# Optimization experiments

Hardware: AMD Instinct MI355X
Metric: run time of the kernel (lower is better)

## Reference

```python
import jax, jax.numpy as jnp
import numpy as np
import math

D_MODEL = 1024
N_HEADS = 16
SPARSITY = 0.3


def setup_inputs() -> dict:
    key = jax.random.key(0)
    ks = jax.random.split(key, 12)
    B, S, D = 4, 2048, D_MODEL
    Dh = D // 2
    sc = 0.02
    inp = {
        "x": jax.random.normal(ks[0], (B, S, D), dtype=jnp.float32),
        "wq": jax.random.normal(ks[1], (D, D), dtype=jnp.float32) * sc,
        "bq": jnp.zeros((D,), jnp.float32),
        "wk": jax.random.normal(ks[2], (D, D), dtype=jnp.float32) * sc,
        "bk": jnp.zeros((D,), jnp.float32),
        "wv": jax.random.normal(ks[3], (D, D), dtype=jnp.float32) * sc,
        "bv": jnp.zeros((D,), jnp.float32),
        "wo": jax.random.normal(ks[4], (D, D), dtype=jnp.float32) * sc,
        "bo": jnp.zeros((D,), jnp.float32),
        "wi1": jax.random.normal(ks[5], (Dh, D), dtype=jnp.float32) * sc,
        "bi1": jnp.zeros((Dh,), jnp.float32),
        "wi2": jax.random.normal(ks[6], (1, Dh), dtype=jnp.float32) * sc,
        "bi2": jnp.zeros((1,), jnp.float32),
    }
    return inp


def reference(x, wq, bq, wk, bk, wv, bv, wo, bo, wi1, bi1, wi2, bi2):
    B, S, D = x.shape
    H = N_HEADS
    hd = D // H
    k = max(1, int(S * SPARSITY))

    # projections (torch Linear: x @ W^T + b)
    Q = (x @ wq.T + bq).reshape(B, S, H, hd).transpose(0, 2, 1, 3)  # [B,H,S,hd]
    K = (x @ wk.T + bk).reshape(B, S, H, hd).transpose(0, 2, 1, 3)
    V = (x @ wv.T + bv).reshape(B, S, H, hd).transpose(0, 2, 1, 3)

    # learned indexer -> per-position importance [B,S]
    h = jnp.maximum(x @ wi1.T + bi1, 0.0)
    importance = (h @ wi2.T + bi2)[..., 0]

    _, top_idx = jax.lax.top_k(importance, k)  # [B,k]
    sparse_mask = jnp.zeros((B, S), dtype=x.dtype).at[
        jnp.arange(B)[:, None], top_idx
    ].set(1.0)

    scores = jnp.einsum("bhqd,bhkd->bhqk", Q, K) / math.sqrt(hd)
    scores = jnp.where(sparse_mask[:, None, None, :] == 0, -jnp.inf, scores)
    attn = jax.nn.softmax(scores, axis=-1)

    out = jnp.einsum("bhqk,bhkd->bhqd", attn, V)
    out = out.transpose(0, 2, 1, 3).reshape(B, S, D)
    return out @ wo.T + bo
```

## Files before the change

kernel.cpp:

```cpp
#include <hip/hip_runtime.h>
#include <math.h>

#define BB 4
#define SS 2048
#define DD 1024
#define HHD 16
#define HD 64
#define DH 512
#define KSEL 614
#define KPAD 640
#define MTOT (BB*SS)
#define QKVS 3072
#define NCH (KPAD/64)

typedef __attribute__((ext_vector_type(8))) short bf16x8;
typedef __attribute__((ext_vector_type(4))) float f32x4;

#define LDS_CAST(p) ((__attribute__((address_space(3))) void*)(p))
#define GLB_CAST(p) ((const __attribute__((address_space(1))) void*)(p))

__device__ inline short bf16rne(float v)
{
    unsigned u = __builtin_bit_cast(unsigned, v);
    return (short)((u + 0x7FFFu + ((u >> 16) & 1u)) >> 16);
}

__device__ inline void split1(float v, short& h, short& l)
{
    unsigned u = __builtin_bit_cast(unsigned, v);
    unsigned hr = (u + 0x7FFFu + ((u >> 16) & 1u)) >> 16;
    h = (short)hr;
    float hf = __builtin_bit_cast(float, hr << 16);
    float res = v - hf;
    unsigned u2 = __builtin_bit_cast(unsigned, res);
    unsigned lr = (u2 + 0x7FFFu + ((u2 >> 16) & 1u)) >> 16;
    l = (short)lr;
}

__global__ __launch_bounds__(256)
void split_convert(const float* __restrict__ in, short* __restrict__ hi,
                   short* __restrict__ lo, int n4)
{
    const int i = blockIdx.x * 256 + threadIdx.x;
    if (i >= n4) return;
    float4 v = reinterpret_cast<const float4*>(in)[i];
    short4 h, l;
    split1(v.x, h.x, l.x);
    split1(v.y, h.y, l.y);
    split1(v.z, h.z, l.z);
    split1(v.w, h.w, l.w);
    reinterpret_cast<short4*>(hi)[i] = h;
    reinterpret_cast<short4*>(lo)[i] = l;
}

__global__ __launch_bounds__(256)
void split_weights(const float* __restrict__ wq, const float* __restrict__ wk,
                   const float* __restrict__ wv, const float* __restrict__ wo,
                   const float* __restrict__ wi1,
                   short* __restrict__ Bqkv_hi, short* __restrict__ wo_hi,
                   short* __restrict__ Wi_hi, short* __restrict__ Wi_lo)
{
    const int i = blockIdx.x * 256 + threadIdx.x;
    const int which = blockIdx.y;
    if (which < 4) {
        const float* src = (which == 0) ? wq : (which == 1) ? wk : (which == 2) ? wv : wo;
        short* dst = (which == 3) ? wo_hi : (Bqkv_hi + (size_t)which * DD * DD);
        float4 v = reinterpret_cast<const float4*>(src)[i];
        short4 hh;
        hh.x = bf16rne(v.x); hh.y = bf16rne(v.y); hh.z = bf16rne(v.z); hh.w = bf16rne(v.w);
        reinterpret_cast<short4*>(dst)[i] = hh;
    } else {
        if (i >= DH*DD/4) return;
        float4 v = reinterpret_cast<const float4*>(wi1)[i];
        short4 h, l;
        split1(v.x, h.x, l.x); split1(v.y, h.y, l.y);
        split1(v.z, h.z, l.z); split1(v.w, h.w, l.w);
        reinterpret_cast<short4*>(Wi_hi)[i] = h;
        reinterpret_cast<short4*>(Wi_lo)[i] = l;
    }
}

__global__ __launch_bounds__(256)
void concat_bias3(const float* __restrict__ a, const float* __restrict__ b,
                  const float* __restrict__ c, float* __restrict__ o)
{
    const int i = blockIdx.x * 256 + threadIdx.x;
    o[i] = (i < 1024) ? a[i] : ((i < 2048) ? b[i - 1024] : c[i - 2048]);
}

template<bool BF16_OUT, bool QSCALE>
__global__ __launch_bounds__(256)
void gemm_bf16(const short* __restrict__ Ahi, const short* __restrict__ Bhi,
               const float* __restrict__ bias, void* __restrict__ Cv,
               int M, int N, int K, int ldc)
{
    __shared__ short sAh[128*64];
    __shared__ short sBh[128*64];

    const int t = threadIdx.x;
    const int lane = t & 63, wid = t >> 6;
    const int wm = wid >> 1, wn = wid & 1;
    const int row0 = blockIdx.y * 128, col0 = blockIdx.x * 128;
    const int g = lane >> 4, r = lane & 15;
    const int lrow = lane >> 3;
    const int lslot = lane & 7;

    f32x4 acc[4][4];
    #pragma unroll
    for (int mt = 0; mt < 4; ++mt)
        #pragma unroll
        for (int nt = 0; nt < 4; ++nt) acc[mt][nt] = (f32x4){0.f, 0.f, 0.f, 0.f};

    for (int k0 = 0; k0 < K; k0 += 64) {
        #pragma unroll
        for (int e = 0; e < 4; ++e) {
            const int rl = wid * 32 + e * 8 + lrow;
            const int scol = k0 + ((lslot ^ (rl & 7)) << 3);
            const size_t ga = (size_t)(row0 + rl) * K + scol;
            const size_t gb = (size_t)(col0 + rl) * K + scol;
            const int ldso = (wid * 32 + e * 8) * 64;
            __builtin_amdgcn_global_load_lds(GLB_CAST(Ahi + ga), LDS_CAST(sAh + ldso), 16, 0, 0);
            __builtin_amdgcn_global_load_lds(GLB_CAST(Bhi + gb), LDS_CAST(sBh + ldso), 16, 0, 0);
        }
        __syncthreads();

        #pragma unroll
        for (int kk = 0; kk < 2; ++kk) {
            bf16x8 ah[4], bh[4];
            #pragma unroll
            for (int mt = 0; mt < 4; ++mt) {
                const int rw = wm * 64 + mt * 16 + r;
                ah[mt] = *reinterpret_cast<const bf16x8*>(sAh + rw * 64 + (((kk*4 + g) ^ (rw & 7)) << 3));
            }
            #pragma unroll
            for (int nt = 0; nt < 4; ++nt) {
                const int rw = wn * 64 + nt * 16 + r;
                bh[nt] = *reinterpret_cast<const bf16x8*>(sBh + rw * 64 + (((kk*4 + g) ^ (rw & 7)) << 3));
            }
            #pragma unroll
            for (int mt = 0; mt < 4; ++mt)
                #pragma unroll
                for (int nt = 0; nt < 4; ++nt)
                    acc[mt][nt] = __builtin_amdgcn_mfma_f32_16x16x32_bf16(ah[mt], bh[nt], acc[mt][nt], 0, 0, 0);
        }
        __syncthreads();
    }

    #pragma unroll
    for (int nt = 0; nt < 4; ++nt) {
        const int col = wn * 64 + nt * 16 + r;
        const float bv = bias[col0 + col];
        const bool qs = QSCALE && (col0 + col) < 1024;
        #pragma unroll
        for (int mt = 0; mt < 4; ++mt) {
            #pragma unroll
            for (int e = 0; e < 4; ++e) {
                const int row = row0 + wm * 64 + mt * 16 + 4 * g + e;
                float v = acc[mt][nt][e] + bv;
                if (qs) v *= 0.125f;
                if (BF16_OUT)
                    ((short*)Cv)[(size_t)row * ldc + col0 + col] = bf16rne(v);
                else
                    ((float*)Cv)[(size_t)row * ldc + col0 + col] = v;
            }
        }
    }
}

template<bool RELU>
__global__ __launch_bounds__(256)
void gemm_split(const short* __restrict__ Ahi, const short* __restrict__ Alo,
                const short* __restrict__ Bhi, const short* __restrict__ Blo,
                const float* __restrict__ bias, float* __restrict__ C,
                int M, int N, int K, int ldc)
{
    __shared__ short sAh[128*32];
    __shared__ short sAl[128*32];
    __shared__ short sBh[128*32];
    __shared__ short sBl[128*32];

    const int t = threadIdx.x;
    const int lane = t & 63, wid = t >> 6;
    const int wm = wid >> 1, wn = wid & 1;
    const int row0 = blockIdx.y * 128, col0 = blockIdx.x * 128;
    const int g = lane >> 4, r = lane & 15;
    const int sw = g ^ ((lane >> 2) & 3);
    const int srow = lane >> 2;
    const int sslot = lane & 3;

    f32x4 acc[4][4];
    #pragma unroll
    for (int mt = 0; mt < 4; ++mt)
        #pragma unroll
        for (int nt = 0; nt < 4; ++nt) acc[mt][nt] = (f32x4){0.f, 0.f, 0.f, 0.f};

    for (int k0 = 0; k0 < K; k0 += 32) {
        #pragma unroll
        for (int i = 0; i < 2; ++i) {
            const int rl = wid * 32 + i * 16 + srow;
            const int scol = k0 + ((sslot ^ ((rl >> 2) & 3)) << 3);
            const size_t ga = (size_t)(row0 + rl) * K + scol;
            const size_t gb = (size_t)(col0 + rl) * K + scol;
            const int ldso = (wid * 32 + i * 16) * 32;
            __builtin_amdgcn_global_load_lds(GLB_CAST(Ahi + ga), LDS_CAST(sAh + ldso), 16, 0, 0);
            __builtin_amdgcn_global_load_lds(GLB_CAST(Alo + ga), LDS_CAST(sAl + ldso), 16, 0, 0);
            __builtin_amdgcn_global_load_lds(GLB_CAST(Bhi + gb), LDS_CAST(sBh + ldso), 16, 0, 0);
            __builtin_amdgcn_global_load_lds(GLB_CAST(Blo + gb), LDS_CAST(sBl + ldso), 16, 0, 0);
        }
        __syncthreads();

        bf16x8 ah[4], al[4], bh[4], bl[4];
        #pragma unroll
        for (int mt = 0; mt < 4; ++mt) {
            const int row = wm * 64 + mt * 16 + r;
            ah[mt] = *reinterpret_cast<const bf16x8*>(sAh + row * 32 + sw * 8);
            al[mt] = *reinterpret_cast<const bf16x8*>(sAl + row * 32 + sw * 8);
        }
        #pragma unroll
        for (int nt = 0; nt < 4; ++nt) {
            const int row = wn * 64 + nt * 16 + r;
            bh[nt] = *reinterpret_cast<const bf16x8*>(sBh + row * 32 + sw * 8);
            bl[nt] = *reinterpret_cast<const bf16x8*>(sBl + row * 32 + sw * 8);
        }
        #pragma unroll
        for (int mt = 0; mt < 4; ++mt)
            #pragma unroll
            for (int nt = 0; nt < 4; ++nt) {
                acc[mt][nt] = __builtin_amdgcn_mfma_f32_16x16x32_bf16(ah[mt], bh[nt], acc[mt][nt], 0, 0, 0);
                acc[mt][nt] = __builtin_amdgcn_mfma_f32_16x16x32_bf16(ah[mt], bl[nt], acc[mt][nt], 0, 0, 0);
                acc[mt][nt] = __builtin_amdgcn_mfma_f32_16x16x32_bf16(al[mt], bh[nt], acc[mt][nt], 0, 0, 0);
            }
        __syncthreads();
    }

    #pragma unroll
    for (int nt = 0; nt < 4; ++nt) {
        const int col = wn * 64 + nt * 16 + r;
        const float bv = bias[col0 + col];
        #pragma unroll
        for (int mt = 0; mt < 4; ++mt) {
            #pragma unroll
            for (int e = 0; e < 4; ++e) {
                const int row = row0 + wm * 64 + mt * 16 + 4 * g + e;
                float v = acc[mt][nt][e] + bv;
                if (RELU) v = fmaxf(v, 0.f);
                C[(size_t)row * ldc + col0 + col] = v;
            }
        }
    }
}

__global__ __launch_bounds__(256)
void importance_kernel(const float* __restrict__ h, const float* __restrict__ wi2,
                       const float* __restrict__ bi2, float* __restrict__ imp)
{
    const int wid = threadIdx.x >> 6, lane = threadIdx.x & 63;
    const int row = blockIdx.x * 4 + wid;
    const float* hr = h + (size_t)row * DH;
    float s = 0.f;
    #pragma unroll
    for (int i = 0; i < DH/64; ++i)
        s = fmaf(hr[lane + i*64], wi2[lane + i*64], s);
    #pragma unroll
    for (int off = 32; off; off >>= 1) s += __shfl_down(s, off);
    if (lane == 0) imp[row] = s + bi2[0];
}

__global__ __launch_bounds__(256)
void rank_kernel(const float* __restrict__ imp, int* __restrict__ flags)
{
    __shared__ float simp[SS];
    const int b = blockIdx.y;
    const int t = threadIdx.x;
    const float* bimp = imp + b * SS;
    for (int i = t; i < SS/4; i += 256)
        reinterpret_cast<float4*>(simp)[i] = reinterpret_cast<const float4*>(bimp)[i];
    __syncthreads();

    const int i = blockIdx.x * 32 + (t >> 3);
    const int part = t & 7;
    const float v = simp[i];
    const float4* slice = reinterpret_cast<const float4*>(simp + part * (SS/8));
    const int jb = part * (SS/8);
    int rank = 0;
    #pragma unroll 8
    for (int jj = 0; jj < SS/32; ++jj) {
        const float4 u4 = slice[jj];
        const int j = jb + jj * 4;
        rank += (u4.x > v) || ((u4.x == v) && (j + 0 < i));
        rank += (u4.y > v) || ((u4.y == v) && (j + 1 < i));
        rank += (u4.z > v) || ((u4.z == v) && (j + 2 < i));
        rank += (u4.w > v) || ((u4.w == v) && (j + 3 < i));
    }
    rank += __shfl_xor(rank, 1);
    rank += __shfl_xor(rank, 2);
    rank += __shfl_xor(rank, 4);
    if (part == 0) flags[b * SS + i] = (rank < KSEL) ? 1 : 0;
}

__global__ __launch_bounds__(256)
void compact_kernel(const int* __restrict__ flags, int* __restrict__ idxg)
{
    __shared__ int sscan[SS];
    __shared__ int sidx[KSEL];
    const int b = blockIdx.x, t = threadIdx.x;
    for (int i = t; i < SS; i += 256) sscan[i] = flags[b * SS + i];
    __syncthreads();
    for (int off = 1; off < SS; off <<= 1) {
        int vals[SS/256];
        #pragma unroll
        for (int c = 0; c < SS/256; ++c) {
            const int i = t + c * 256;
            int v = sscan[i];
            if (i >= off) v += sscan[i - off];
            vals[c] = v;
        }
        __syncthreads();
        #pragma unroll
        for (int c = 0; c < SS/256; ++c) sscan[t + c * 256] = vals[c];
        __syncthreads();
    }
    for (int i = t; i < SS; i += 256) {
        const int f = flags[b * SS + i];
        if (f) sidx[sscan[i] - 1] = i;
    }
    __syncthreads();
    for (int p = t; p < KPAD; p += 256)
        idxg[b * KPAD + p] = sidx[min(p, KSEL - 1)];
}

__global__ __launch_bounds__(256)
void gather_kv(const short* __restrict__ QKVb, const int* __restrict__ idxg,
               short* __restrict__ Kg, short* __restrict__ Vg)
{
    __shared__ short Vs[64*72];
    const int t = threadIdx.x;
    const int c = blockIdx.x, h = blockIdx.y, b = blockIdx.z;
    const int srow = t >> 2;
    const int sq4  = t & 3;

    const size_t cbase = ((size_t)(b * HHD + h) * NCH + c) * 4096;

    const int krow = idxg[b * KPAD + c * 64 + srow];
    const short* kb = QKVb + (size_t)(b * SS + krow) * QKVS + 1024 + h * HD + sq4 * 16;
    bf16x8 k0 = *reinterpret_cast<const bf16x8*>(kb);
    bf16x8 k1 = *reinterpret_cast<const bf16x8*>(kb + 8);
    short* kout = Kg + cbase + srow * HD + sq4 * 16;
    *reinterpret_cast<bf16x8*>(kout)     = k0;
    *reinterpret_cast<bf16x8*>(kout + 8) = k1;

    const short* vbp = kb + 1024;
    bf16x8 v0 = *reinterpret_cast<const bf16x8*>(vbp);
    bf16x8 v1 = *reinterpret_cast<const bf16x8*>(vbp + 8);
    #pragma unroll
    for (int j = 0; j < 8; ++j) {
        Vs[(sq4 * 16 + j) * 72 + srow]     = v0[j];
        Vs[(sq4 * 16 + 8 + j) * 72 + srow] = v1[j];
    }
    __syncthreads();

    const int x = 8 * (srow >> 4);
    short* vout = Vg + cbase + srow * 64;
    *reinterpret_cast<bf16x8*>(vout + ((sq4 * 16)     ^ x)) = *reinterpret_cast<const bf16x8*>(&Vs[srow * 72 + sq4 * 16]);
    *reinterpret_cast<bf16x8*>(vout + ((sq4 * 16 + 8) ^ x)) = *reinterpret_cast<const bf16x8*>(&Vs[srow * 72 + sq4 * 16 + 8]);
}

__global__ __launch_bounds__(256)
void attn_mfma(const short* __restrict__ QKVb, const short* __restrict__ Kg,
               const short* __restrict__ Vg, short* __restrict__ AOhi)
{
    __shared__ short Ks[2][64*72];
    __shared__ short Vs[2][64*72];
    __shared__ short Ps[4][16*72];

    const int t = threadIdx.x;
    const int lane = t & 63, w = t >> 6;
    const int g = lane >> 4, r = lane & 15;
    const int qt = blockIdx.x, h = blockIdx.y, b = blockIdx.z;
    const int q0 = qt * 64;
    short* Psw = &Ps[w][0];

    const int srow = t >> 2;
    const int scol = (t & 3) * 16;
    const short* kcbase = Kg + ((size_t)(b * HHD + h) * NCH) * 4096 + srow * 64 + scol;
    const short* vcbase = Vg + ((size_t)(b * HHD + h) * NCH) * 4096 + srow * 64 + scol;

    bf16x8 qh[2];
    {
        const short* qrow = QKVb + (size_t)(b * SS + q0 + w * 16 + r) * QKVS + h * HD;
        qh[0] = *reinterpret_cast<const bf16x8*>(qrow + 8 * g);
        qh[1] = *reinterpret_cast<const bf16x8*>(qrow + 32 + 8 * g);
    }

    bf16x8 ones;
    #pragma unroll
    for (int j = 0; j < 8; ++j) ones[j] = (short)0x3F80;

    f32x4 oacc[4];
    #pragma unroll
    for (int dt = 0; dt < 4; ++dt) oacc[dt] = (f32x4){0.f, 0.f, 0.f, 0.f};
    f32x4 dacc = (f32x4){0.f, 0.f, 0.f, 0.f};

    bf16x8 kreg0 = *reinterpret_cast<const bf16x8*>(kcbase);
    bf16x8 kreg1 = *reinterpret_cast<const bf16x8*>(kcbase + 8);
    bf16x8 vreg0 = *reinterpret_cast<const bf16x8*>(vcbase);
    bf16x8 vreg1 = *reinterpret_cast<const bf16x8*>(vcbase + 8);

    for (int c = 0; c < NCH; ++c) {
        const int cur = c & 1;
        *reinterpret_cast<bf16x8*>(&Ks[cur][srow*72 + scol])     = kreg0;
        *reinterpret_cast<bf16x8*>(&Ks[cur][srow*72 + scol + 8]) = kreg1;
        *reinterpret_cast<bf16x8*>(&Vs[cur][srow*72 + scol])     = vreg0;
        *reinterpret_cast<bf16x8*>(&Vs[cur][srow*72 + scol + 8]) = vreg1;
        if (c + 1 < NCH) {
            const short* kn = kcbase + (size_t)(c + 1) * 4096;
            const short* vn = vcbase + (size_t)(c + 1) * 4096;
            kreg0 = *reinterpret_cast<const bf16x8*>(kn);
            kreg1 = *reinterpret_cast<const bf16x8*>(kn + 8);
            vreg0 = *reinterpret_cast<const bf16x8*>(vn);
            vreg1 = *reinterpret_cast<const bf16x8*>(vn + 8);
        }
        __syncthreads();

        f32x4 sa[4];
        #pragma unroll
        for (int kt = 0; kt < 4; ++kt) {
            bf16x8 kf0 = *reinterpret_cast<const bf16x8*>(&Ks[cur][(kt*16 + r)*72 + 8*g]);
            bf16x8 kf1 = *reinterpret_cast<const bf16x8*>(&Ks[cur][(kt*16 + r)*72 + 32 + 8*g]);
            f32x4 s = (f32x4){0.f, 0.f, 0.f, 0.f};
            s = __builtin_amdgcn_mfma_f32_16x16x32_bf16(qh[0], kf0, s, 0, 0, 0);
            s = __builtin_amdgcn_mfma_f32_16x16x32_bf16(qh[1], kf1, s, 0, 0, 0);
            sa[kt] = s;
        }
        if (c == NCH - 1) {
            #pragma unroll
            for (int kt = 0; kt < 4; ++kt)
                if (c*64 + kt*16 + r >= KSEL)
                    sa[kt] = (f32x4){-INFINITY, -INFINITY, -INFINITY, -INFINITY};
        }

        #pragma unroll
        for (int kt = 0; kt < 4; ++kt)
            #pragma unroll
            for (int e = 0; e < 4; ++e)
                Psw[(4*g + e)*72 + ((kt*16 + r) ^ (8*g))] = bf16rne(__expf(sa[kt][e]));

        #pragma unroll
        for (int kc = 0; kc < 2; ++kc) {
            bf16x8 pf = *reinterpret_cast<const bf16x8*>(&Psw[r*72 + kc*32 + 8*(g ^ (r >> 2))]);
            dacc = __builtin_amdgcn_mfma_f32_16x16x32_bf16(pf, ones, dacc, 0, 0, 0);
            #pragma unroll
            for (int dt = 0; dt < 4; ++dt) {
                bf16x8 vf = *reinterpret_cast<const bf16x8*>(&Vs[cur][(dt*16 + r)*72 + kc*32 + 8*(g ^ dt)]);
                oacc[dt] = __builtin_amdgcn_mfma_f32_16x16x32_bf16(pf, vf, oacc[dt], 0, 0, 0);
            }
        }
    }

    #pragma unroll
    for (int dt = 0; dt < 4; ++dt)
        #pragma unroll
        for (int e = 0; e < 4; ++e) {
            const size_t a = (size_t)(b * SS + q0 + w*16 + 4*g + e) * DD + h * HD + dt*16 + r;
            AOhi[a] = bf16rne(oacc[dt][e] / dacc[e]);
        }
}

extern "C" void kernel_launch(void* const* d_in, const int* in_sizes, int n_in,
                              void* d_out, int out_size, void* d_ws, size_t ws_size,
                              hipStream_t stream)
{
    const float* x   = (const float*)d_in[0];
    const float* wq  = (const float*)d_in[1];
    const float* bq  = (const float*)d_in[2];
    const float* wk  = (const float*)d_in[3];
    const float* bk  = (const float*)d_in[4];
    const float* wv  = (const float*)d_in[5];
    const float* bv  = (const float*)d_in[6];
    const float* wo  = (const float*)d_in[7];
    const float* bo  = (const float*)d_in[8];
    const float* wi1 = (const float*)d_in[9];
    const float* bi1 = (const float*)d_in[10];
    const float* wi2 = (const float*)d_in[11];
    const float* bi2 = (const float*)d_in[12];
    float* out = (float*)d_out;

    const size_t MB = 1ull << 20;
    char* W = (char*)d_ws;
    short* x_hi  = (short*)(W + 0);
    short* x_lo  = (short*)(W + 16*MB);
    short* QKVb  = (short*)(W + 32*MB);
    short* Bqkv_hi=(short*)(W + 128*MB);
    short* wo_hi = (short*)(W + 134*MB);
    float* Hw    = (float*)(W + 144*MB);
    float* bqkv  = (float*)(W + 160*MB);
    float* imp   = (float*)(W + 160*MB + 64*1024);
    int*   flags = (int*)(W + 160*MB + 128*1024);
    int*   idxg  = (int*)(W + 160*MB + 192*1024);
    short* Wi_hi = (short*)(W + 96*MB);
    short* Wi_lo = (short*)(W + 97*MB);
    short* Kg = (short*)(W + 144*MB);
    short* Vg = (short*)(W + 150*MB);
    short* AO_hi = x_hi;

    const size_t NM = (size_t)MTOT * DD;

    split_convert<<<(NM/4 + 255)/256, 256, 0, stream>>>(x, x_hi, x_lo, NM/4);
    split_weights<<<dim3(DD*DD/4/256, 5), 256, 0, stream>>>(
        wq, wk, wv, wo, wi1, Bqkv_hi, wo_hi, Wi_hi, Wi_lo);
    concat_bias3<<<QKVS/256, 256, 0, stream>>>(bq, bk, bv, bqkv);

    gemm_split<true><<<dim3(DH/128, MTOT/128), 256, 0, stream>>>(
        x_hi, x_lo, Wi_hi, Wi_lo, bi1, Hw, MTOT, DH, DD, DH);
    importance_kernel<<<MTOT/4, 256, 0, stream>>>(Hw, wi2, bi2, imp);
    rank_kernel<<<dim3(SS/32, BB), 256, 0, stream>>>(imp, flags);
    compact_kernel<<<BB, 256, 0, stream>>>(flags, idxg);

    gemm_bf16<true, true><<<dim3(QKVS/128, MTOT/128), 256, 0, stream>>>(
        x_hi, Bqkv_hi, bqkv, QKVb, MTOT, QKVS, DD, QKVS);

    gather_kv<<<dim3(NCH, HHD, BB), 256, 0, stream>>>(QKVb, idxg, Kg, Vg);

    attn_mfma<<<dim3(SS/64, HHD, BB), 256, 0, stream>>>(QKVb, Kg, Vg, AO_hi);

    gemm_bf16<false, false><<<dim3(DD/128, MTOT/128), 256, 0, stream>>>(
        AO_hi, wo_hi, bo, out, MTOT, DD, DD, DD);
}
```

Baseline: 230.7 us.

## Compute K/V projections only for top-k selected rows via gathered GEMM

Splits the fused QKV projection into a full Q GEMM and a K/V GEMM that gathers only the selected key positions through the index list. K/V projection work over unselected rows is skipped, and the projected-activation buffer shrinks. The gather_kv kernel now reads from the compact K/V buffer. In exchange, the A-operand loads are indirect row gathers, and the K/V GEMM must wait for the top-k selection.

```diff
diff --git a/kernel.cpp b/kernel.cpp
--- a/kernel.cpp
+++ b/kernel.cpp
@@ -10,8 +10,8 @@
 #define KSEL 614
 #define KPAD 640
 #define MTOT (BB*SS)
-#define QKVS 3072
 #define NCH (KPAD/64)
+#define MKV (BB*KPAD)
 
 typedef __attribute__((ext_vector_type(8))) short bf16x8;
 typedef __attribute__((ext_vector_type(4))) float f32x4;
@@ -81,11 +81,11 @@
 }
 
 __global__ __launch_bounds__(256)
-void concat_bias3(const float* __restrict__ a, const float* __restrict__ b,
-                  const float* __restrict__ c, float* __restrict__ o)
+void concat_bias2(const float* __restrict__ a, const float* __restrict__ b,
+                  float* __restrict__ o)
 {
     const int i = blockIdx.x * 256 + threadIdx.x;
-    o[i] = (i < 1024) ? a[i] : ((i < 2048) ? b[i - 1024] : c[i - 2048]);
+    o[i] = (i < 1024) ? a[i] : b[i - 1024];
 }
 
 template<bool BF16_OUT, bool QSCALE>
@@ -162,6 +162,86 @@
                     ((short*)Cv)[(size_t)row * ldc + col0 + col] = bf16rne(v);
                 else
                     ((float*)Cv)[(size_t)row * ldc + col0 + col] = v;
+            }
+        }
+    }
+}
+
+__global__ __launch_bounds__(256)
+void gemm_kv_gather(const short* __restrict__ Ahi, const short* __restrict__ Bhi,
+                    const int* __restrict__ idxg, const float* __restrict__ bias,
+                    short* __restrict__ C)
+{
+    __shared__ short sAh[128*64];
+    __shared__ short sBh[128*64];
+
+    const int K = DD, N = 2048;
+    const int t = threadIdx.x;
+    const int lane = t & 63, wid = t >> 6;
+    const int wm = wid >> 1, wn = wid & 1;
+    const int row0 = blockIdx.y * 128, col0 = blockIdx.x * 128;
+    const int g = lane >> 4, r = lane & 15;
+    const int lrow = lane >> 3;
+    const int lslot = lane & 7;
+
+    size_t garow[4];
+    #pragma unroll
+    for (int e = 0; e < 4; ++e) {
+        const int rl = row0 + wid * 32 + e * 8 + lrow;
+        const int grow = (rl / KPAD) * SS + idxg[rl];
+        garow[e] = (size_t)grow * K;
+    }
+
+    f32x4 acc[4][4];
+    #pragma unroll
+    for (int mt = 0; mt < 4; ++mt)
+        #pragma unroll
+        for (int nt = 0; nt < 4; ++nt) acc[mt][nt] = (f32x4){0.f, 0.f, 0.f, 0.f};
+
+    for (int k0 = 0; k0 < K; k0 += 64) {
+        #pragma unroll
+        for (int e = 0; e < 4; ++e) {
+            const int rl = wid * 32 + e * 8 + lrow;
+            const int scol = k0 + ((lslot ^ (rl & 7)) << 3);
+            const size_t gb = (size_t)(col0 + rl) * K + scol;
+            const int ldso = (wid * 32 + e * 8) * 64;
+            __builtin_amdgcn_global_load_lds(GLB_CAST(Ahi + garow[e] + scol), LDS_CAST(sAh + ldso), 16, 0, 0);
+            __builtin_amdgcn_global_load_lds(GLB_CAST(Bhi + gb), LDS_CAST(sBh + ldso), 16, 0, 0);
+        }
+        __syncthreads();
+
+        #pragma unroll
+        for (int kk = 0; kk < 2; ++kk) {
+            bf16x8 ah[4], bh[4];
+            #pragma unroll
+            for (int mt = 0; mt < 4; ++mt) {
+                const int rw = wm * 64 + mt * 16 + r;
+                ah[mt] = *reinterpret_cast<const bf16x8*>(sAh + rw * 64 + (((kk*4 + g) ^ (rw & 7)) << 3));
+            }
+            #pragma unroll
+            for (int nt = 0; nt < 4; ++nt) {
+                const int rw = wn * 64 + nt * 16 + r;
+                bh[nt] = *reinterpret_cast<const bf16x8*>(sBh + rw * 64 + (((kk*4 + g) ^ (rw & 7)) << 3));
+            }
+            #pragma unroll
+            for (int mt = 0; mt < 4; ++mt)
+                #pragma unroll
+                for (int nt = 0; nt < 4; ++nt)
+                    acc[mt][nt] = __builtin_amdgcn_mfma_f32_16x16x32_bf16(ah[mt], bh[nt], acc[mt][nt], 0, 0, 0);
+        }
+        __syncthreads();
+    }
+
+    #pragma unroll
+    for (int nt = 0; nt < 4; ++nt) {
+        const int col = wn * 64 + nt * 16 + r;
+        const float bv = bias[col0 + col];
+        #pragma unroll
+        for (int mt = 0; mt < 4; ++mt) {
+            #pragma unroll
+            for (int e = 0; e < 4; ++e) {
+                const int row = row0 + wm * 64 + mt * 16 + 4 * g + e;
+                C[(size_t)row * N + col0 + col] = bf16rne(acc[mt][nt][e] + bv);
             }
         }
     }
@@ -330,8 +410,8 @@
 }
 
 __global__ __launch_bounds__(256)
-void gather_kv(const short* __restrict__ QKVb, const int* __restrict__ idxg,
-               short* __restrict__ Kg, short* __restrict__ Vg)
+void gather_kv(const short* __restrict__ KVc, short* __restrict__ Kg,
+               short* __restrict__ Vg)
 {
     __shared__ short Vs[64*72];
     const int t = threadIdx.x;
@@ -341,8 +421,7 @@
 
     const size_t cbase = ((size_t)(b * HHD + h) * NCH + c) * 4096;
 
-    const int krow = idxg[b * KPAD + c * 64 + srow];
-    const short* kb = QKVb + (size_t)(b * SS + krow) * QKVS + 1024 + h * HD + sq4 * 16;
+    const short* kb = KVc + (size_t)(b * KPAD + c * 64 + srow) * 2048 + h * HD + sq4 * 16;
     bf16x8 k0 = *reinterpret_cast<const bf16x8*>(kb);
     bf16x8 k1 = *reinterpret_cast<const bf16x8*>(kb + 8);
     short* kout = Kg + cbase + srow * HD + sq4 * 16;
@@ -366,7 +445,7 @@
 }
 
 __global__ __launch_bounds__(256)
-void attn_mfma(const short* __restrict__ QKVb, const short* __restrict__ Kg,
+void attn_mfma(const short* __restrict__ Qb, const short* __restrict__ Kg,
                const short* __restrict__ Vg, short* __restrict__ AOhi)
 {
     __shared__ short Ks[2][64*72];
@@ -387,7 +466,7 @@
 
     bf16x8 qh[2];
     {
-        const short* qrow = QKVb + (size_t)(b * SS + q0 + w * 16 + r) * QKVS + h * HD;
+        const short* qrow = Qb + (size_t)(b * SS + q0 + w * 16 + r) * DD + h * HD;
         qh[0] = *reinterpret_cast<const bf16x8*>(qrow + 8 * g);
         qh[1] = *reinterpret_cast<const bf16x8*>(qrow + 32 + 8 * g);
     }
@@ -489,18 +568,19 @@
     char* W = (char*)d_ws;
     short* x_hi  = (short*)(W + 0);
     short* x_lo  = (short*)(W + 16*MB);
-    short* QKVb  = (short*)(W + 32*MB);
+    short* Qb    = (short*)(W + 32*MB);
+    short* KVc   = (short*)(W + 48*MB);
+    short* Wi_hi = (short*)(W + 96*MB);
+    short* Wi_lo = (short*)(W + 97*MB);
     short* Bqkv_hi=(short*)(W + 128*MB);
     short* wo_hi = (short*)(W + 134*MB);
     float* Hw    = (float*)(W + 144*MB);
-    float* bqkv  = (float*)(W + 160*MB);
+    short* Kg    = (short*)(W + 144*MB);
+    short* Vg    = (short*)(W + 150*MB);
+    float* bkv   = (float*)(W + 160*MB);
     float* imp   = (float*)(W + 160*MB + 64*1024);
     int*   flags = (int*)(W + 160*MB + 128*1024);
     int*   idxg  = (int*)(W + 160*MB + 192*1024);
-    short* Wi_hi = (short*)(W + 96*MB);
-    short* Wi_lo = (short*)(W + 97*MB);
-    short* Kg = (short*)(W + 144*MB);
-    short* Vg = (short*)(W + 150*MB);
     short* AO_hi = x_hi;
 
     const size_t NM = (size_t)MTOT * DD;
@@ -508,7 +588,7 @@
     split_convert<<<(NM/4 + 255)/256, 256, 0, stream>>>(x, x_hi, x_lo, NM/4);
     split_weights<<<dim3(DD*DD/4/256, 5), 256, 0, stream>>>(
         wq, wk, wv, wo, wi1, Bqkv_hi, wo_hi, Wi_hi, Wi_lo);
-    concat_bias3<<<QKVS/256, 256, 0, stream>>>(bq, bk, bv, bqkv);
+    concat_bias2<<<2048/256, 256, 0, stream>>>(bk, bv, bkv);
 
     gemm_split<true><<<dim3(DH/128, MTOT/128), 256, 0, stream>>>(
         x_hi, x_lo, Wi_hi, Wi_lo, bi1, Hw, MTOT, DH, DD, DH);
@@ -516,12 +596,14 @@
     rank_kernel<<<dim3(SS/32, BB), 256, 0, stream>>>(imp, flags);
     compact_kernel<<<BB, 256, 0, stream>>>(flags, idxg);
 
-    gemm_bf16<true, true><<<dim3(QKVS/128, MTOT/128), 256, 0, stream>>>(
-        x_hi, Bqkv_hi, bqkv, QKVb, MTOT, QKVS, DD, QKVS);
-
-    gather_kv<<<dim3(NCH, HHD, BB), 256, 0, stream>>>(QKVb, idxg, Kg, Vg);
-
-    attn_mfma<<<dim3(SS/64, HHD, BB), 256, 0, stream>>>(QKVb, Kg, Vg, AO_hi);
+    gemm_bf16<true, true><<<dim3(DD/128, MTOT/128), 256, 0, stream>>>(
+        x_hi, Bqkv_hi, bq, Qb, MTOT, DD, DD, DD);
+    gemm_kv_gather<<<dim3(2048/128, MKV/128), 256, 0, stream>>>(
+        x_hi, Bqkv_hi + (size_t)DD*DD, idxg, bkv, KVc);
+
+    gather_kv<<<dim3(NCH, HHD, BB), 256, 0, stream>>>(KVc, Kg, Vg);
+
+    attn_mfma<<<dim3(SS/64, HHD, BB), 256, 0, stream>>>(Qb, Kg, Vg, AO_hi);
 
     gemm_bf16<false, false><<<dim3(DD/128, MTOT/128), 256, 0, stream>>>(
         AO_hi, wo_hi, bo, out, MTOT, DD, DD, DD);
```

After: 211.5 us. 8.3% less time.
